# Performance work log

Measured on AMD Instinct MI355X. Metric: run time of the kernel, lower is better.

Reference implementation:

```python
import jax, jax.numpy as jnp
import numpy as np

N_NODES = 50000
N_EDGES = 800000
F_IN = 128
F_HID = 128
N_CLS = 1
E_TR = 100000
E_TE = 20000


def setup_inputs() -> dict:
    key = jax.random.key(0)
    ks = jax.random.split(key, 16)
    inp = {
        'x': jax.random.normal(ks[0], (N_NODES, F_IN), dtype=jnp.float32),
        'edge_index': jax.random.randint(ks[1], (2, N_EDGES), 0, N_NODES, dtype=jnp.int32),
        'pos_edges_train': jax.random.randint(ks[2], (2, E_TR), 0, N_NODES, dtype=jnp.int32),
        'neg_edges_train': jax.random.randint(ks[3], (2, E_TR), 0, N_NODES, dtype=jnp.int32),
        'pos_edges_test': jax.random.randint(ks[4], (2, E_TE), 0, N_NODES, dtype=jnp.int32),
        'neg_edges_test': jax.random.randint(ks[5], (2, E_TE), 0, N_NODES, dtype=jnp.int32),
    }
    s = 0.05
    inp['W0'] = jax.random.normal(ks[6], (F_IN, F_HID), dtype=jnp.float32) * s
    inp['b0'] = jnp.zeros((F_HID,), dtype=jnp.float32)
    inp['W1'] = jax.random.normal(ks[7], (F_HID, F_HID), dtype=jnp.float32) * s
    inp['b1'] = jnp.zeros((F_HID,), dtype=jnp.float32)
    inp['W2'] = jax.random.normal(ks[8], (F_HID, F_HID), dtype=jnp.float32) * s
    inp['b2'] = jnp.zeros((F_HID,), dtype=jnp.float32)
    inp['W3'] = jax.random.normal(ks[9], (F_HID, F_HID), dtype=jnp.float32) * s
    inp['b3'] = jnp.zeros((F_HID,), dtype=jnp.float32)
    inp['Wl1'] = jax.random.normal(ks[10], (2 * F_HID, F_HID), dtype=jnp.float32) * s
    inp['bl1'] = jnp.zeros((F_HID,), dtype=jnp.float32)
    inp['Wl2'] = jax.random.normal(ks[11], (F_HID, N_CLS), dtype=jnp.float32) * s
    inp['bl2'] = jnp.zeros((N_CLS,), dtype=jnp.float32)
    return inp


def _gcn_conv(h, W, b, src, dst, dis):
    # PyG GCNConv: out = D^{-1/2}(A+I)D^{-1/2} (h W) + b, with self loops folded in analytically
    hw = h @ W                                           # [N, F]
    msg = hw[src] * dis[src][:, None]                    # [E, F]
    agg = jax.ops.segment_sum(msg, dst, num_segments=N_NODES)
    return agg * dis[:, None] + hw * (dis ** 2)[:, None] + b


def _edge_feats(x, e):
    return jnp.concatenate([x[e[0]], x[e[1]]], axis=1)


def reference(x, edge_index, pos_edges_train, neg_edges_train, pos_edges_test, neg_edges_test,
              W0, b0, W1, b1, W2, b2, W3, b3, Wl1, bl1, Wl2, bl2):
    src, dst = edge_index[0], edge_index[1]
    # degree with self loop (+1), symmetric normalization
    deg = jax.ops.segment_sum(jnp.ones((src.shape[0],), jnp.float32), dst, num_segments=N_NODES) + 1.0
    dis = deg ** -0.5

    h = jax.nn.relu(_gcn_conv(x, W0, b0, src, dst, dis))
    h = jax.nn.relu(_gcn_conv(h, W1, b1, src, dst, dis))
    h = jax.nn.relu(_gcn_conv(h, W2, b2, src, dst, dis))
    h = _gcn_conv(h, W3, b3, src, dst, dis)

    x_train = jnp.concatenate([_edge_feats(h, pos_edges_train), _edge_feats(h, neg_edges_train)], axis=0)
    x_test = jnp.concatenate([_edge_feats(h, pos_edges_test), _edge_feats(h, neg_edges_test)], axis=0)
    n_train = x_train.shape[0]
    z = jnp.concatenate([x_train, x_test], axis=0)
    z = jax.nn.relu(z @ Wl1 + bl1)
    z = (z @ Wl2 + bl2).squeeze(1)
    return (z[:n_train], z[n_train:])
```

## Files before the change

### kernel.cpp

```cpp
#include <hip/hip_runtime.h>
#include <math.h>

#define NN 50000
#define NE 800000
#define FD 128
#define SCAN_B 196
#define NTR 100000
#define NTE 20000


__global__ __launch_bounds__(256) void k_zero_int(int* __restrict__ p, int n) {
    int i = blockIdx.x * 256 + threadIdx.x;
    if (i < n) p[i] = 0;
}

__global__ __launch_bounds__(256) void k_count(const int* __restrict__ dst, int* __restrict__ deg) {
    int e = blockIdx.x * 256 + threadIdx.x;
    if (e < NE) atomicAdd(&deg[dst[e]], 1);
}


__global__ __launch_bounds__(256) void k_scan1(const int* __restrict__ deg,
                                               int* __restrict__ partial,
                                               int* __restrict__ bsum,
                                               float* __restrict__ dis) {
    __shared__ int wsum[4];
    const int t = threadIdx.x, lane = t & 63, wid = t >> 6;
    const int i = blockIdx.x * 256 + t;
    int v = (i < NN) ? deg[i] : 0;
    int sc = v;
#pragma unroll
    for (int d = 1; d < 64; d <<= 1) {
        int o = __shfl_up(sc, d, 64);
        if (lane >= d) sc += o;
    }
    if (lane == 63) wsum[wid] = sc;
    __syncthreads();
    int pre = 0;
    for (int w = 0; w < wid; ++w) pre += wsum[w];
    if (i < NN) {
        partial[i] = pre + sc - v;
        dis[i] = (float)(1.0 / sqrt((double)(v + 1)));
    }
    if (t == 255) bsum[blockIdx.x] = pre + sc;
}

__global__ __launch_bounds__(256) void k_scan2(int* __restrict__ bsum) {
    __shared__ int wsum[4];
    const int t = threadIdx.x, lane = t & 63, wid = t >> 6;
    int v = (t < SCAN_B) ? bsum[t] : 0;
    int sc = v;
#pragma unroll
    for (int d = 1; d < 64; d <<= 1) {
        int o = __shfl_up(sc, d, 64);
        if (lane >= d) sc += o;
    }
    if (lane == 63) wsum[wid] = sc;
    __syncthreads();
    int pre = 0;
    for (int w = 0; w < wid; ++w) pre += wsum[w];
    if (t < SCAN_B) bsum[t] = pre + sc - v;
}

__global__ __launch_bounds__(256) void k_scan3(const int* __restrict__ partial,
                                               const int* __restrict__ bsum,
                                               int* __restrict__ offs,
                                               int* __restrict__ cursor) {
    const int i = blockIdx.x * 256 + threadIdx.x;
    if (i < NN) {
        int o = partial[i] + bsum[blockIdx.x];
        offs[i] = o;
        cursor[i] = o;
    }
    if (i == 0) offs[NN] = NE;
}


__global__ __launch_bounds__(256) void k_fill(const int* __restrict__ src, const int* __restrict__ dst,
                                              int* __restrict__ cursor, int* __restrict__ srcs_sorted) {
    int e = blockIdx.x * 256 + threadIdx.x;
    if (e < NE) {
        int d = dst[e];
        int p = atomicAdd(&cursor[d], 1);
        srcs_sorted[p] = src[e];
    }
}


__global__ __launch_bounds__(256) void k_gemm(const float* __restrict__ A,
                                              const float* __restrict__ W,
                                              const float* __restrict__ dis,
                                              float* __restrict__ C, int nrows) {
    __shared__ float As[32][128];
    const int t = threadIdx.x;
    const int row0 = blockIdx.x * 32;

    for (int idx = t; idx < 32 * 32; idx += 256) {
        int r = idx >> 5, c = idx & 31;
        float4 v = make_float4(0.f, 0.f, 0.f, 0.f);
        if (row0 + r < nrows)
            v = reinterpret_cast<const float4*>(A)[(size_t)(row0 + r) * 32 + c];
        reinterpret_cast<float4*>(&As[r][0])[c] = v;
    }
    __syncthreads();

    const int cg = t & 31;
    const int eg = t >> 5;
    float acc[4][4] = {{0.f}};

    const float4* W4 = reinterpret_cast<const float4*>(W);
    const float4* As4 = reinterpret_cast<const float4*>(As);

    float4 w0 = W4[0 * 32 + cg];
    float4 w1 = W4[1 * 32 + cg];
    float4 w2 = W4[2 * 32 + cg];
    float4 w3 = W4[3 * 32 + cg];

    for (int k4 = 0; k4 < 32; ++k4) {
        int kn = (k4 < 31) ? (k4 + 1) : 31;
        float4 n0 = W4[(kn * 4 + 0) * 32 + cg];
        float4 n1 = W4[(kn * 4 + 1) * 32 + cg];
        float4 n2 = W4[(kn * 4 + 2) * 32 + cg];
        float4 n3 = W4[(kn * 4 + 3) * 32 + cg];
#pragma unroll
        for (int i = 0; i < 4; ++i) {
            float4 a = As4[(eg * 4 + i) * 32 + k4];
            acc[i][0] += a.x * w0.x + a.y * w1.x + a.z * w2.x + a.w * w3.x;
            acc[i][1] += a.x * w0.y + a.y * w1.y + a.z * w2.y + a.w * w3.y;
            acc[i][2] += a.x * w0.z + a.y * w1.z + a.z * w2.z + a.w * w3.z;
            acc[i][3] += a.x * w0.w + a.y * w1.w + a.z * w2.w + a.w * w3.w;
        }
        w0 = n0; w1 = n1; w2 = n2; w3 = n3;
    }

#pragma unroll
    for (int i = 0; i < 4; ++i) {
        int r = row0 + eg * 4 + i;
        if (r < nrows) {
            float d = dis[r];
            float4 o = make_float4(acc[i][0] * d, acc[i][1] * d, acc[i][2] * d, acc[i][3] * d);
            reinterpret_cast<float4*>(C)[(size_t)r * 32 + cg] = o;
        }
    }
}


__global__ __launch_bounds__(256) void k_gemm_pair(const float* __restrict__ A,
                                                   const float* __restrict__ Wa,
                                                   const float* __restrict__ Wb,
                                                   float* __restrict__ U,
                                                   float* __restrict__ V, int nrows) {
    __shared__ float As[32][128];
    const int t = threadIdx.x;
    const int row0 = blockIdx.x * 32;
    const float* W = (blockIdx.y == 0) ? Wa : Wb;
    float* C = (blockIdx.y == 0) ? U : V;

    for (int idx = t; idx < 32 * 32; idx += 256) {
        int r = idx >> 5, c = idx & 31;
        float4 v = make_float4(0.f, 0.f, 0.f, 0.f);
        if (row0 + r < nrows)
            v = reinterpret_cast<const float4*>(A)[(size_t)(row0 + r) * 32 + c];
        reinterpret_cast<float4*>(&As[r][0])[c] = v;
    }
    __syncthreads();

    const int cg = t & 31;
    const int eg = t >> 5;
    float acc[4][4] = {{0.f}};

    const float4* W4 = reinterpret_cast<const float4*>(W);
    const float4* As4 = reinterpret_cast<const float4*>(As);

    float4 w0 = W4[0 * 32 + cg];
    float4 w1 = W4[1 * 32 + cg];
    float4 w2 = W4[2 * 32 + cg];
    float4 w3 = W4[3 * 32 + cg];

    for (int k4 = 0; k4 < 32; ++k4) {
        int kn = (k4 < 31) ? (k4 + 1) : 31;
        float4 n0 = W4[(kn * 4 + 0) * 32 + cg];
        float4 n1 = W4[(kn * 4 + 1) * 32 + cg];
        float4 n2 = W4[(kn * 4 + 2) * 32 + cg];
        float4 n3 = W4[(kn * 4 + 3) * 32 + cg];
#pragma unroll
        for (int i = 0; i < 4; ++i) {
            float4 a = As4[(eg * 4 + i) * 32 + k4];
            acc[i][0] += a.x * w0.x + a.y * w1.x + a.z * w2.x + a.w * w3.x;
            acc[i][1] += a.x * w0.y + a.y * w1.y + a.z * w2.y + a.w * w3.y;
            acc[i][2] += a.x * w0.z + a.y * w1.z + a.z * w2.z + a.w * w3.z;
            acc[i][3] += a.x * w0.w + a.y * w1.w + a.z * w2.w + a.w * w3.w;
        }
        w0 = n0; w1 = n1; w2 = n2; w3 = n3;
    }

#pragma unroll
    for (int i = 0; i < 4; ++i) {
        int r = row0 + eg * 4 + i;
        if (r < nrows) {
            float4 o = make_float4(acc[i][0], acc[i][1], acc[i][2], acc[i][3]);
            reinterpret_cast<float4*>(C)[(size_t)r * 32 + cg] = o;
        }
    }
}


template <bool RELU>
__global__ __launch_bounds__(256) void k_gather(const float* __restrict__ hws,
                                                const float* __restrict__ dis,
                                                const float* __restrict__ b,
                                                const int* __restrict__ offs,
                                                const int* __restrict__ srcs,
                                                float* __restrict__ out) {
    const int t = threadIdx.x;
    const int f4 = t & 31;
    const int node = blockIdx.x * 8 + (t >> 5);
    if (node >= NN) return;

    const float4* H4 = reinterpret_cast<const float4*>(hws);
    float4 acc = H4[(size_t)node * 32 + f4];
    const int e0 = offs[node], e1 = offs[node + 1];
    int e = e0;
    for (; e + 8 <= e1; e += 8) {
        int s0 = srcs[e + 0], s1 = srcs[e + 1], s2 = srcs[e + 2], s3 = srcs[e + 3];
        int s4 = srcs[e + 4], s5 = srcs[e + 5], s6 = srcs[e + 6], s7 = srcs[e + 7];
        float4 v0 = H4[(size_t)s0 * 32 + f4];
        float4 v1 = H4[(size_t)s1 * 32 + f4];
        float4 v2 = H4[(size_t)s2 * 32 + f4];
        float4 v3 = H4[(size_t)s3 * 32 + f4];
        float4 v4 = H4[(size_t)s4 * 32 + f4];
        float4 v5 = H4[(size_t)s5 * 32 + f4];
        float4 v6 = H4[(size_t)s6 * 32 + f4];
        float4 v7 = H4[(size_t)s7 * 32 + f4];
        acc.x += ((v0.x + v1.x) + (v2.x + v3.x)) + ((v4.x + v5.x) + (v6.x + v7.x));
        acc.y += ((v0.y + v1.y) + (v2.y + v3.y)) + ((v4.y + v5.y) + (v6.y + v7.y));
        acc.z += ((v0.z + v1.z) + (v2.z + v3.z)) + ((v4.z + v5.z) + (v6.z + v7.z));
        acc.w += ((v0.w + v1.w) + (v2.w + v3.w)) + ((v4.w + v5.w) + (v6.w + v7.w));
    }
    for (; e < e1; ++e) {
        int s = srcs[e];
        float4 v = H4[(size_t)s * 32 + f4];
        acc.x += v.x; acc.y += v.y; acc.z += v.z; acc.w += v.w;
    }
    float d = dis[node];
    float4 bb = reinterpret_cast<const float4*>(b)[f4];
    float4 o;
    o.x = acc.x * d + bb.x;
    o.y = acc.y * d + bb.y;
    o.z = acc.z * d + bb.z;
    o.w = acc.w * d + bb.w;
    if (RELU) {
        o.x = fmaxf(o.x, 0.f); o.y = fmaxf(o.y, 0.f);
        o.z = fmaxf(o.z, 0.f); o.w = fmaxf(o.w, 0.f);
    }
    reinterpret_cast<float4*>(out)[(size_t)node * 32 + f4] = o;
}


__global__ __launch_bounds__(256) void k_edge_score(const float* __restrict__ U,
                                                    const float* __restrict__ V,
                                                    const int* __restrict__ tp,
                                                    const int* __restrict__ tn,
                                                    const int* __restrict__ sp,
                                                    const int* __restrict__ sn,
                                                    const float* __restrict__ bl1,
                                                    const float* __restrict__ Wl2,
                                                    const float* __restrict__ bl2,
                                                    float* __restrict__ out) {
    const int t = threadIdx.x;
    const int f4 = t & 31;
    const int e = blockIdx.x * 8 + (t >> 5);
    if (e >= 2 * NTR + 2 * NTE) return;

    int a, bn;
    if (e < NTR)                { a = tp[e];              bn = tp[e + NTR]; }
    else if (e < 2 * NTR)       { a = tn[e - NTR];        bn = tn[e]; }
    else if (e < 2 * NTR + NTE) { a = sp[e - 2 * NTR];    bn = sp[e - 2 * NTR + NTE]; }
    else                        { a = sn[e - 2 * NTR - NTE]; bn = sn[e - 2 * NTR]; }

    float4 u = reinterpret_cast<const float4*>(U)[(size_t)a * 32 + f4];
    float4 v = reinterpret_cast<const float4*>(V)[(size_t)bn * 32 + f4];
    float4 bb = reinterpret_cast<const float4*>(bl1)[f4];
    float4 w2 = reinterpret_cast<const float4*>(Wl2)[f4];

    float s = fmaxf(u.x + v.x + bb.x, 0.f) * w2.x
            + fmaxf(u.y + v.y + bb.y, 0.f) * w2.y
            + fmaxf(u.z + v.z + bb.z, 0.f) * w2.z
            + fmaxf(u.w + v.w + bb.w, 0.f) * w2.w;
#pragma unroll
    for (int m = 16; m >= 1; m >>= 1) s += __shfl_xor(s, m, 64);
    if (f4 == 0) out[e] = s + bl2[0];
}


extern "C" void kernel_launch(void* const* d_in, const int* in_sizes, int n_in,
                              void* d_out, int out_size, void* d_ws, size_t ws_size,
                              hipStream_t stream) {
    const float* x = (const float*)d_in[0];
    const int* ei = (const int*)d_in[1];
    const int* srcp = ei;
    const int* dstp = ei + NE;

    const int* e_tr_pos = (const int*)d_in[2];
    const int* e_tr_neg = (const int*)d_in[3];
    const int* e_te_pos = (const int*)d_in[4];
    const int* e_te_neg = (const int*)d_in[5];

    const float* W[4] = {(const float*)d_in[6], (const float*)d_in[8],
                         (const float*)d_in[10], (const float*)d_in[12]};
    const float* b[4] = {(const float*)d_in[7], (const float*)d_in[9],
                         (const float*)d_in[11], (const float*)d_in[13]};
    const float* Wl1 = (const float*)d_in[14];
    const float* bl1 = (const float*)d_in[15];
    const float* Wl2 = (const float*)d_in[16];
    const float* bl2 = (const float*)d_in[17];

    float* ws = (float*)d_ws;
    float* dis = ws;
    int* deg = (int*)(ws + 50176);
    int* offs = (int*)(ws + 100352);
    int* cursor = (int*)(ws + 150784);
    int* bsum = (int*)(ws + 200960);
    int* srcs = (int*)(ws + 201216);
    float* B0 = ws + 1001216;
    float* B1 = B0 + 6400000;
    float* B2 = B1 + 6400000;
    int* partial = (int*)B2;

    k_zero_int<<<(NN + 255) / 256, 256, 0, stream>>>(deg, NN);
    k_count<<<(NE + 255) / 256, 256, 0, stream>>>(dstp, deg);
    k_scan1<<<SCAN_B, 256, 0, stream>>>(deg, partial, bsum, dis);
    k_scan2<<<1, 256, 0, stream>>>(bsum);
    k_scan3<<<SCAN_B, 256, 0, stream>>>(partial, bsum, offs, cursor);
    k_fill<<<(NE + 255) / 256, 256, 0, stream>>>(srcp, dstp, cursor, srcs);

    const int gemm_blocks = (NN + 31) / 32;
    const int gath_blocks = (NN + 7) / 8;

    float* hout[4] = {B1, B2, B1, B2};
    const float* hin = x;
    for (int l = 0; l < 4; ++l) {
        k_gemm<<<gemm_blocks, 256, 0, stream>>>(hin, W[l], dis, B0, NN);
        if (l < 3)
            k_gather<true><<<gath_blocks, 256, 0, stream>>>(B0, dis, b[l], offs, srcs, hout[l]);
        else
            k_gather<false><<<gath_blocks, 256, 0, stream>>>(B0, dis, b[l], offs, srcs, hout[l]);
        hin = hout[l];
    }

    const float* hfin = B2;
    float* Ubuf = B0;
    float* Vbuf = B1;
    k_gemm_pair<<<dim3(gemm_blocks, 2), 256, 0, stream>>>(hfin, Wl1, Wl1 + 128 * 128,
                                                          Ubuf, Vbuf, NN);

    float* out = (float*)d_out;
    const int n_all = 2 * NTR + 2 * NTE;
    k_edge_score<<<(n_all + 7) / 8, 256, 0, stream>>>(Ubuf, Vbuf,
                                                      e_tr_pos, e_tr_neg, e_te_pos, e_te_neg,
                                                      bl1, Wl2, bl2, out);
}
```

Baseline: 572.6 us.

## Fuse neighbor gather of each GCN layer with the next layer's GEMM

Adds a fused kernel that aggregates neighbor features for 32 nodes into shared memory, applies bias and ReLU, then multiplies by the next layer's weight and scales by dis. The intermediate hidden activations no longer make a round trip through global memory between layers 1-3, and three kernel launches go away. In exchange each block does the gather with 32 nodes per block at 4-way unrolling instead of 8 nodes per block at 8-way, which may reduce latency hiding and occupancy for the memory-bound gather.

```diff
diff --git a/kernel.cpp b/kernel.cpp
--- a/kernel.cpp
+++ b/kernel.cpp
@@ -140,6 +140,96 @@
             float d = dis[r];
             float4 o = make_float4(acc[i][0] * d, acc[i][1] * d, acc[i][2] * d, acc[i][3] * d);
             reinterpret_cast<float4*>(C)[(size_t)r * 32 + cg] = o;
+        }
+    }
+}
+
+
+__global__ __launch_bounds__(256) void k_fused_gg(const float* __restrict__ hws_in,
+                                                  const float* __restrict__ dis,
+                                                  const float* __restrict__ bprev,
+                                                  const float* __restrict__ W,
+                                                  const int* __restrict__ offs,
+                                                  const int* __restrict__ srcs,
+                                                  float* __restrict__ hws_out, int nrows) {
+    __shared__ float As[32][128];
+    const int t = threadIdx.x;
+    const int f4 = t & 31;
+    const int ng = t >> 5;
+    const int row0 = blockIdx.x * 32;
+
+    const float4* H4 = reinterpret_cast<const float4*>(hws_in);
+    float4 bb = reinterpret_cast<const float4*>(bprev)[f4];
+
+    for (int nl = ng; nl < 32; nl += 8) {
+        int node = row0 + nl;
+        float4 o = make_float4(0.f, 0.f, 0.f, 0.f);
+        if (node < nrows) {
+            float4 acc = H4[(size_t)node * 32 + f4];
+            const int e0 = offs[node], e1 = offs[node + 1];
+            int e = e0;
+            for (; e + 4 <= e1; e += 4) {
+                int s0 = srcs[e + 0], s1 = srcs[e + 1], s2 = srcs[e + 2], s3 = srcs[e + 3];
+                float4 v0 = H4[(size_t)s0 * 32 + f4];
+                float4 v1 = H4[(size_t)s1 * 32 + f4];
+                float4 v2 = H4[(size_t)s2 * 32 + f4];
+                float4 v3 = H4[(size_t)s3 * 32 + f4];
+                acc.x += (v0.x + v1.x) + (v2.x + v3.x);
+                acc.y += (v0.y + v1.y) + (v2.y + v3.y);
+                acc.z += (v0.z + v1.z) + (v2.z + v3.z);
+                acc.w += (v0.w + v1.w) + (v2.w + v3.w);
+            }
+            for (; e < e1; ++e) {
+                int s = srcs[e];
+                float4 v = H4[(size_t)s * 32 + f4];
+                acc.x += v.x; acc.y += v.y; acc.z += v.z; acc.w += v.w;
+            }
+            float d = dis[node];
+            o.x = fmaxf(acc.x * d + bb.x, 0.f);
+            o.y = fmaxf(acc.y * d + bb.y, 0.f);
+            o.z = fmaxf(acc.z * d + bb.z, 0.f);
+            o.w = fmaxf(acc.w * d + bb.w, 0.f);
+        }
+        reinterpret_cast<float4*>(&As[nl][0])[f4] = o;
+    }
+    __syncthreads();
+
+    const int cg = f4;
+    const int eg = ng;
+    float acc[4][4] = {{0.f}};
+
+    const float4* W4 = reinterpret_cast<const float4*>(W);
+    const float4* As4 = reinterpret_cast<const float4*>(As);
+
+    float4 w0 = W4[0 * 32 + cg];
+    float4 w1 = W4[1 * 32 + cg];
+    float4 w2 = W4[2 * 32 + cg];
+    float4 w3 = W4[3 * 32 + cg];
+
+    for (int k4 = 0; k4 < 32; ++k4) {
+        int kn = (k4 < 31) ? (k4 + 1) : 31;
+        float4 n0 = W4[(kn * 4 + 0) * 32 + cg];
+        float4 n1 = W4[(kn * 4 + 1) * 32 + cg];
+        float4 n2 = W4[(kn * 4 + 2) * 32 + cg];
+        float4 n3 = W4[(kn * 4 + 3) * 32 + cg];
+#pragma unroll
+        for (int i = 0; i < 4; ++i) {
+            float4 a = As4[(eg * 4 + i) * 32 + k4];
+            acc[i][0] += a.x * w0.x + a.y * w1.x + a.z * w2.x + a.w * w3.x;
+            acc[i][1] += a.x * w0.y + a.y * w1.y + a.z * w2.y + a.w * w3.y;
+            acc[i][2] += a.x * w0.z + a.y * w1.z + a.z * w2.z + a.w * w3.z;
+            acc[i][3] += a.x * w0.w + a.y * w1.w + a.z * w2.w + a.w * w3.w;
+        }
+        w0 = n0; w1 = n1; w2 = n2; w3 = n3;
+    }
+
+#pragma unroll
+    for (int i = 0; i < 4; ++i) {
+        int r = row0 + eg * 4 + i;
+        if (r < nrows) {
+            float d = dis[r];
+            float4 o = make_float4(acc[i][0] * d, acc[i][1] * d, acc[i][2] * d, acc[i][3] * d);
+            reinterpret_cast<float4*>(hws_out)[(size_t)r * 32 + cg] = o;
         }
     }
 }
@@ -205,13 +295,12 @@
 }
 
 
-template <bool RELU>
-__global__ __launch_bounds__(256) void k_gather(const float* __restrict__ hws,
-                                                const float* __restrict__ dis,
-                                                const float* __restrict__ b,
-                                                const int* __restrict__ offs,
-                                                const int* __restrict__ srcs,
-                                                float* __restrict__ out) {
+__global__ __launch_bounds__(256) void k_gather_f(const float* __restrict__ hws,
+                                                  const float* __restrict__ dis,
+                                                  const float* __restrict__ b,
+                                                  const int* __restrict__ offs,
+                                                  const int* __restrict__ srcs,
+                                                  float* __restrict__ out) {
     const int t = threadIdx.x;
     const int f4 = t & 31;
     const int node = blockIdx.x * 8 + (t >> 5);
@@ -249,10 +338,6 @@
     o.y = acc.y * d + bb.y;
     o.z = acc.z * d + bb.z;
     o.w = acc.w * d + bb.w;
-    if (RELU) {
-        o.x = fmaxf(o.x, 0.f); o.y = fmaxf(o.y, 0.f);
-        o.z = fmaxf(o.z, 0.f); o.w = fmaxf(o.w, 0.f);
-    }
     reinterpret_cast<float4*>(out)[(size_t)node * 32 + f4] = o;
 }
 
@@ -337,21 +422,14 @@
     const int gemm_blocks = (NN + 31) / 32;
     const int gath_blocks = (NN + 7) / 8;
 
-    float* hout[4] = {B1, B2, B1, B2};
-    const float* hin = x;
-    for (int l = 0; l < 4; ++l) {
-        k_gemm<<<gemm_blocks, 256, 0, stream>>>(hin, W[l], dis, B0, NN);
-        if (l < 3)
-            k_gather<true><<<gath_blocks, 256, 0, stream>>>(B0, dis, b[l], offs, srcs, hout[l]);
-        else
-            k_gather<false><<<gath_blocks, 256, 0, stream>>>(B0, dis, b[l], offs, srcs, hout[l]);
-        hin = hout[l];
-    }
-
-    const float* hfin = B2;
+    k_gemm<<<gemm_blocks, 256, 0, stream>>>(x, W[0], dis, B0, NN);
+    k_fused_gg<<<gemm_blocks, 256, 0, stream>>>(B0, dis, b[0], W[1], offs, srcs, B1, NN);
+    k_fused_gg<<<gemm_blocks, 256, 0, stream>>>(B1, dis, b[1], W[2], offs, srcs, B0, NN);
+    k_fused_gg<<<gemm_blocks, 256, 0, stream>>>(B0, dis, b[2], W[3], offs, srcs, B1, NN);
+    k_gather_f<<<gath_blocks, 256, 0, stream>>>(B1, dis, b[3], offs, srcs, B2);
     float* Ubuf = B0;
     float* Vbuf = B1;
-    k_gemm_pair<<<dim3(gemm_blocks, 2), 256, 0, stream>>>(hfin, Wl1, Wl1 + 128 * 128,
+    k_gemm_pair<<<dim3(gemm_blocks, 2), 256, 0, stream>>>(B2, Wl1, Wl1 + 128 * 128,
                                                           Ubuf, Vbuf, NN);
 
     float* out = (float*)d_out;
```

Measured after the change: 541.8 us. 5.4% less time.
